# Kernel optimization log

Hardware: AMD Instinct MI355X
Metric: run time of the kernel (lower is better)

Reference implementation:

```python
import jax, jax.numpy as jnp
import numpy as np

NUM_EMBEDDINGS = 1024
EMBEDDING_DIM = 64
COMMITMENT_COST = 0.25

def setup_inputs() -> dict:
    key = jax.random.key(0)
    k1, k2 = jax.random.split(key)
    z = jax.random.normal(k1, (64, EMBEDDING_DIM, 32, 32), dtype=jnp.float32)
    # nn.Embedding initialized uniform(-1/K, 1/K)
    lim = 1.0 / NUM_EMBEDDINGS
    embeddings = jax.random.uniform(k2, (NUM_EMBEDDINGS, EMBEDDING_DIM), dtype=jnp.float32, minval=-lim, maxval=lim)
    return {"z": z, "embeddings": embeddings}

def reference(z, embeddings):
    # z: [B, C, H, W] with C == embedding_dim
    z_perm = jnp.transpose(z, (0, 2, 3, 1))            # [B, H, W, D]
    flat_z = z_perm.reshape(-1, EMBEDDING_DIM)          # [N, D]
    # squared L2 distances: ||z||^2 - 2 z.e + ||e||^2  -> [N, K]
    distances = (jnp.sum(flat_z ** 2, axis=1, keepdims=True)
                 - 2.0 * flat_z @ embeddings.T
                 + jnp.sum(embeddings ** 2, axis=1))
    encoding_indices = jnp.argmin(distances, axis=1)    # [N]
    # direct gather == one-hot @ embeddings (same math, no [N,K] one-hot)
    quantized = embeddings[encoding_indices].reshape(z_perm.shape)
    commitment_loss = COMMITMENT_COST * jnp.mean((jax.lax.stop_gradient(quantized) - z_perm) ** 2)
    codebook_loss = jnp.mean((quantized - jax.lax.stop_gradient(z_perm)) ** 2)
    loss = commitment_loss + codebook_loss
    # straight-through estimator
    quantized_st = z_perm + jax.lax.stop_gradient(quantized - z_perm)
    return jnp.transpose(quantized_st, (0, 3, 1, 2)), loss
```

## Files before the change

### kernel.cpp

```cpp
#include <hip/hip_runtime.h>

#define D 64
#define K 1024
#define NVEC 65536
#define MB 64
#define NBLK (NVEC / MB)
#define WAVES 4
#define KPW (K / WAVES)
#define TILES (KPW / 16)
#define NG (MB / 16)

typedef __attribute__((ext_vector_type(8))) short bf16x8;
typedef __attribute__((ext_vector_type(4))) float f32x4;

__device__ inline unsigned pk2t(float a, float b) {
    return __builtin_amdgcn_perm(__builtin_bit_cast(unsigned, b),
                                 __builtin_bit_cast(unsigned, a), 0x07060302u);
}
__device__ inline int max3i(int a, int b, int c) {
    const int m = a > b ? a : b;
    return m > c ? m : c;
}

__global__ __launch_bounds__(256) void vq_prep(const float* __restrict__ emb,
                                               unsigned* __restrict__ ebf_u,
                                               float* __restrict__ hb) {
    const int r = blockIdx.x * 8 + (threadIdx.x >> 5);
    const int j = threadIdx.x & 31;
    const float2 v = *reinterpret_cast<const float2*>(emb + (size_t)r * D + j * 2);
    ebf_u[(size_t)r * 32 + j] = pk2t(v.x, v.y);
    float s = fmaf(v.x, v.x, v.y * v.y);
#pragma unroll
    for (int off = 1; off < 32; off <<= 1) s += __shfl_xor(s, off, 64);
    if (j == 0) hb[r] = 1.0f - 0.5f * s;
}

__global__ __launch_bounds__(256, 4) void vq_main(const float* __restrict__ z,
                                                  const float* __restrict__ emb,
                                                  const unsigned short* __restrict__ ebf,
                                                  const float* __restrict__ hb,
                                                  float* __restrict__ out,
                                                  float* __restrict__ pP) {
    __shared__ __align__(16) char zl[MB * 128];
    __shared__ int   wv[WAVES * MB];
    __shared__ int   fin[MB];
    __shared__ float red[256];

    const int tid = threadIdx.x;
    const int blk = blockIdx.x;
    const int b   = blk >> 4;
    const int hw0 = (blk & 15) * MB;
    const float* zb = z + (size_t)b * (D * 1024) + hw0;

    const int wave = tid >> 6;
    const int lane = tid & 63;
    const int cw   = wave * KPW;

    float zacc = 0.f;
    {
        const int v4 = tid & 15;
        const int d4 = tid >> 4;
        float4 r[4];
#pragma unroll
        for (int i = 0; i < 4; ++i)
            r[i] = *reinterpret_cast<const float4*>(zb + (size_t)(d4 * 4 + i) * 1024 + v4 * 4);
        const float* rf = reinterpret_cast<const float*>(r);
#pragma unroll
        for (int n = 0; n < 16; ++n) zacc = fmaf(rf[n], rf[n], zacc);
#pragma unroll
        for (int j = 0; j < 4; ++j) {
            const int v = v4 * 4 + j;
            uint2 pk;
            pk.x = pk2t(rf[0 * 4 + j], rf[1 * 4 + j]);
            pk.y = pk2t(rf[2 * 4 + j], rf[3 * 4 + j]);
            const int byte = v * 128 + ((d4 * 8) ^ ((v & 7) << 4));
            *reinterpret_cast<uint2*>(zl + byte) = pk;
        }
    }
    __syncthreads();

    const int l16 = lane & 15;
    const int lg  = lane >> 4;

    bf16x8 bfr[NG][2];
#pragma unroll
    for (int g = 0; g < NG; ++g)
#pragma unroll
        for (int h = 0; h < 2; ++h) {
            const int v = g * 16 + l16;
            const int byte = v * 128 + (((h * 64) + lg * 16) ^ ((v & 7) << 4));
            bfr[g][h] = *reinterpret_cast<const bf16x8*>(zl + byte);
        }

    int best[NG];
#pragma unroll
    for (int g = 0; g < NG; ++g) best[g] = 0;

    bf16x8 a0 = *reinterpret_cast<const bf16x8*>(ebf + (size_t)(cw + l16) * 64 + lg * 8);
    bf16x8 a1 = *reinterpret_cast<const bf16x8*>(ebf + (size_t)(cw + l16) * 64 + 32 + lg * 8);
    f32x4  ci = *reinterpret_cast<const f32x4*>(hb + cw + lg * 4);

#pragma unroll 2
    for (int kt = 0; kt < TILES; ++kt) {
        const bf16x8 b0 = a0, b1 = a1;
        const f32x4  cc = ci;
        const int nk = (kt + 1 < TILES) ? kt + 1 : TILES - 1;
        const unsigned short* nrow = ebf + (size_t)(cw + nk * 16 + l16) * 64;
        a0 = *reinterpret_cast<const bf16x8*>(nrow + lg * 8);
        a1 = *reinterpret_cast<const bf16x8*>(nrow + 32 + lg * 8);
        ci = *reinterpret_cast<const f32x4*>(hb + cw + nk * 16 + lg * 4);

        const int idx0 = cw + kt * 16 + lg * 4;
#pragma unroll
        for (int g = 0; g < NG; ++g) {
            f32x4 c = cc;
            c = __builtin_amdgcn_mfma_f32_16x16x32_bf16(b0, bfr[g][0], c, 0, 0, 0);
            c = __builtin_amdgcn_mfma_f32_16x16x32_bf16(b1, bfr[g][1], c, 0, 0, 0);
            const int p0 = (int)((__builtin_bit_cast(unsigned, c[0]) & 0xFFFFFC00u) | (unsigned)(idx0 + 0));
            const int p1 = (int)((__builtin_bit_cast(unsigned, c[1]) & 0xFFFFFC00u) | (unsigned)(idx0 + 1));
            const int p2 = (int)((__builtin_bit_cast(unsigned, c[2]) & 0xFFFFFC00u) | (unsigned)(idx0 + 2));
            const int p3 = (int)((__builtin_bit_cast(unsigned, c[3]) & 0xFFFFFC00u) | (unsigned)(idx0 + 3));
            best[g] = max3i(max3i(p0, p1, p2), p3, best[g]);
        }
    }

#pragma unroll
    for (int g = 0; g < NG; ++g) {
        int tv = best[g];
        int o = __shfl_xor(tv, 16, 64); tv = tv > o ? tv : o;
        o = __shfl_xor(tv, 32, 64);     tv = tv > o ? tv : o;
        if (lane < 16) wv[wave * MB + g * 16 + l16] = tv;
    }
    __syncthreads();

    float tcon = 0.f;
    if (tid < MB) {
        int tv = wv[tid];
#pragma unroll
        for (int w = 1; w < WAVES; ++w) {
            const int o = wv[w * MB + tid];
            tv = tv > o ? tv : o;
        }
        fin[tid] = tv & (K - 1);
        tcon = __builtin_bit_cast(float, (unsigned)tv & 0xFFFFFC00u) - 1.0f;
    }
    __syncthreads();

    {
        const int v  = tid & 63;
        const int dh = tid >> 6;
        const int idx = fin[v];
        const float4* eq4 = reinterpret_cast<const float4*>(emb + (size_t)idx * D + dh * 16);
        float* ob = out + (size_t)b * (D * 1024) + hw0 + v;
#pragma unroll
        for (int i = 0; i < 4; ++i) {
            const float4 q = eq4[i];
            const int d = dh * 16 + i * 4;
            ob[(size_t)(d + 0) * 1024] = q.x;
            ob[(size_t)(d + 1) * 1024] = q.y;
            ob[(size_t)(d + 2) * 1024] = q.z;
            ob[(size_t)(d + 3) * 1024] = q.w;
        }
    }

    red[tid] = zacc - 2.f * tcon;
    __syncthreads();
#pragma unroll
    for (int s = 128; s > 0; s >>= 1) {
        if (tid < s) red[tid] += red[tid + s];
        __syncthreads();
    }
    if (tid == 0) pP[blk] = red[0];
}

__global__ __launch_bounds__(256) void vq_loss(const float* __restrict__ pP,
                                               float* __restrict__ loss_out) {
    __shared__ float red[256];
    float s = 0.f;
    for (int i = threadIdx.x; i < NBLK; i += 256) s += pP[i];
    red[threadIdx.x] = s;
    __syncthreads();
#pragma unroll
    for (int st = 128; st > 0; st >>= 1) {
        if (threadIdx.x < st) red[threadIdx.x] += red[threadIdx.x + st];
        __syncthreads();
    }
    if (threadIdx.x == 0)
        loss_out[0] = 1.25f * red[0] * (1.0f / (float)((size_t)NVEC * D));
}

extern "C" void kernel_launch(void* const* d_in, const int* in_sizes, int n_in,
                              void* d_out, int out_size, void* d_ws, size_t ws_size,
                              hipStream_t stream) {
    const float* z   = (const float*)d_in[0];
    const float* emb = (const float*)d_in[1];
    float* out = (float*)d_out;

    char* ws = (char*)d_ws;
    unsigned* ebf_u = (unsigned*)ws;
    float* hb = (float*)(ws + 131072);
    float* pP = (float*)(ws + 135168);

    vq_prep<<<128, 256, 0, stream>>>(emb, ebf_u, hb);
    vq_main<<<NBLK, 256, 0, stream>>>(z, emb, (const unsigned short*)ebf_u, hb, out, pP);
    vq_loss<<<1, 256, 0, stream>>>(pP, out + (size_t)NVEC * D);
}
```

Measured before the change: 35.16 us.

## Double vectors per block and prefetch codebook tiles two ahead

Each block now handles 128 vectors instead of 64, so every codebook fragment loaded from global memory feeds twice as many MFMAs, and the grid is halved. The codebook prefetch becomes a two-deep register ring, and the first loads are issued before the LDS barrier to hide latency. Launch bounds drop to 2 blocks per SM to allow the extra bf16 fragments and best-index registers, which reduces occupancy and leaves fewer blocks to spread across CUs.

```diff
diff --git a/kernel.cpp b/kernel.cpp
--- a/kernel.cpp
+++ b/kernel.cpp
@@ -3,7 +3,7 @@
 #define D 64
 #define K 1024
 #define NVEC 65536
-#define MB 64
+#define MB 128
 #define NBLK (NVEC / MB)
 #define WAVES 4
 #define KPW (K / WAVES)
@@ -35,7 +35,7 @@
     if (j == 0) hb[r] = 1.0f - 0.5f * s;
 }
 
-__global__ __launch_bounds__(256, 4) void vq_main(const float* __restrict__ z,
+__global__ __launch_bounds__(256, 2) void vq_main(const float* __restrict__ z,
                                                   const float* __restrict__ emb,
                                                   const unsigned short* __restrict__ ebf,
                                                   const float* __restrict__ hb,
@@ -48,18 +48,22 @@
 
     const int tid = threadIdx.x;
     const int blk = blockIdx.x;
-    const int b   = blk >> 4;
-    const int hw0 = (blk & 15) * MB;
+    const int b   = blk >> 3;
+    const int hw0 = (blk & 7) * MB;
     const float* zb = z + (size_t)b * (D * 1024) + hw0;
 
     const int wave = tid >> 6;
     const int lane = tid & 63;
     const int cw   = wave * KPW;
+    const int l16  = lane & 15;
+    const int lg   = lane >> 4;
 
     float zacc = 0.f;
-    {
-        const int v4 = tid & 15;
-        const int d4 = tid >> 4;
+#pragma unroll
+    for (int it = 0; it < 2; ++it) {
+        const int item = it * 256 + tid;
+        const int v4 = item & 31;
+        const int d4 = item >> 5;
         float4 r[4];
 #pragma unroll
         for (int i = 0; i < 4; ++i)
@@ -77,10 +81,17 @@
             *reinterpret_cast<uint2*>(zl + byte) = pk;
         }
     }
-    __syncthreads();
-
-    const int l16 = lane & 15;
-    const int lg  = lane >> 4;
+
+    bf16x8 A0[2], A1[2];
+    f32x4  CI[2];
+#pragma unroll
+    for (int p = 0; p < 2; ++p) {
+        const unsigned short* row = ebf + (size_t)(cw + p * 16 + l16) * 64;
+        A0[p] = *reinterpret_cast<const bf16x8*>(row + lg * 8);
+        A1[p] = *reinterpret_cast<const bf16x8*>(row + 32 + lg * 8);
+        CI[p] = *reinterpret_cast<const f32x4*>(hb + cw + p * 16 + lg * 4);
+    }
+    __syncthreads();
 
     bf16x8 bfr[NG][2];
 #pragma unroll
@@ -96,19 +107,16 @@
 #pragma unroll
     for (int g = 0; g < NG; ++g) best[g] = 0;
 
-    bf16x8 a0 = *reinterpret_cast<const bf16x8*>(ebf + (size_t)(cw + l16) * 64 + lg * 8);
-    bf16x8 a1 = *reinterpret_cast<const bf16x8*>(ebf + (size_t)(cw + l16) * 64 + 32 + lg * 8);
-    f32x4  ci = *reinterpret_cast<const f32x4*>(hb + cw + lg * 4);
-
 #pragma unroll 2
     for (int kt = 0; kt < TILES; ++kt) {
-        const bf16x8 b0 = a0, b1 = a1;
-        const f32x4  cc = ci;
-        const int nk = (kt + 1 < TILES) ? kt + 1 : TILES - 1;
+        const int cur = kt & 1;
+        const bf16x8 b0 = A0[cur], b1 = A1[cur];
+        const f32x4  cc = CI[cur];
+        const int nk = (kt + 2 < TILES) ? kt + 2 : kt;
         const unsigned short* nrow = ebf + (size_t)(cw + nk * 16 + l16) * 64;
-        a0 = *reinterpret_cast<const bf16x8*>(nrow + lg * 8);
-        a1 = *reinterpret_cast<const bf16x8*>(nrow + 32 + lg * 8);
-        ci = *reinterpret_cast<const f32x4*>(hb + cw + nk * 16 + lg * 4);
+        A0[cur] = *reinterpret_cast<const bf16x8*>(nrow + lg * 8);
+        A1[cur] = *reinterpret_cast<const bf16x8*>(nrow + 32 + lg * 8);
+        CI[cur] = *reinterpret_cast<const f32x4*>(hb + cw + nk * 16 + lg * 4);
 
         const int idx0 = cw + kt * 16 + lg * 4;
 #pragma unroll
@@ -147,15 +155,15 @@
     __syncthreads();
 
     {
-        const int v  = tid & 63;
-        const int dh = tid >> 6;
+        const int v  = tid & 127;
+        const int dh = tid >> 7;
         const int idx = fin[v];
-        const float4* eq4 = reinterpret_cast<const float4*>(emb + (size_t)idx * D + dh * 16);
+        const float4* eq4 = reinterpret_cast<const float4*>(emb + (size_t)idx * D + dh * 32);
         float* ob = out + (size_t)b * (D * 1024) + hw0 + v;
 #pragma unroll
-        for (int i = 0; i < 4; ++i) {
+        for (int i = 0; i < 8; ++i) {
             const float4 q = eq4[i];
-            const int d = dh * 16 + i * 4;
+            const int d = dh * 32 + i * 4;
             ob[(size_t)(d + 0) * 1024] = q.x;
             ob[(size_t)(d + 1) * 1024] = q.y;
             ob[(size_t)(d + 2) * 1024] = q.z;
```

New measurement: 28.30 us. 19.5% less time.
